# Kernel optimization log

Measured on AMD Instinct MI355X. Metric: run time of the kernel, lower is better.

The kernel has to match this reference:

```python
import jax, jax.numpy as jnp
import numpy as np


def setup_inputs() -> dict:
    key = jax.random.key(0)
    x = jax.random.normal(key, (32, 128, 112, 112), dtype=jnp.float32)
    return {"x": x}


def reference(x) -> jnp.ndarray:
    # Max-Feature-Map: pairwise max over adjacent channel pairs.
    # Equivalent to the original loop that takes max(x[:,k], x[:,k+1]) for k in 0,2,...
    B, C, H, W = x.shape
    return x.reshape(B, C // 2, 2, H, W).max(axis=2)  # [B, C/2, H, W]
```

## Files before the change

### kernel.cpp

```cpp
#include <hip/hip_runtime.h>


typedef float f32x4 __attribute__((ext_vector_type(4)));

static constexpr int P4 = (112 * 112) / 4;
static constexpr int N4_OUT = 32 * 64 * P4;

__global__ __launch_bounds__(256) void mfm_kernel(const f32x4* __restrict__ x,
                                                  f32x4* __restrict__ out) {
    int i = blockIdx.x * blockDim.x + threadIdx.x;
    int p = i / P4;
    int in0 = i + p * P4;
    f32x4 a = __builtin_nontemporal_load(&x[in0]);
    f32x4 b = __builtin_nontemporal_load(&x[in0 + P4]);
    f32x4 r;
    r.x = fmaxf(a.x, b.x);
    r.y = fmaxf(a.y, b.y);
    r.z = fmaxf(a.z, b.z);
    r.w = fmaxf(a.w, b.w);
    __builtin_nontemporal_store(r, &out[i]);
}

extern "C" void kernel_launch(void* const* d_in, const int* in_sizes, int n_in,
                              void* d_out, int out_size, void* d_ws, size_t ws_size,
                              hipStream_t stream) {
    const f32x4* x = (const f32x4*)d_in[0];
    f32x4* out = (f32x4*)d_out;
    constexpr int block = 256;
    constexpr int grid = N4_OUT / block;
    mfm_kernel<<<grid, block, 0, stream>>>(x, out);
}
```

Measured before the change: 287.2 us.

## Map one block per output plane with unrolled multi-load per thread

Each block now processes one whole output channel plane, 448 threads each doing seven float4 loads from both input channels before computing and storing. This removes the per-element integer division and gives each thread more loads in flight. The cost is fewer blocks (2048) with a larger register footprint, which may reduce occupancy and latency hiding.

After: 292.3 us. Within noise of the previous version (+1.8%).

```diff
diff --git a/kernel.cpp b/kernel.cpp
--- a/kernel.cpp
+++ b/kernel.cpp
@@ -4,21 +4,35 @@
 typedef float f32x4 __attribute__((ext_vector_type(4)));
 
 static constexpr int P4 = (112 * 112) / 4;
-static constexpr int N4_OUT = 32 * 64 * P4;
+static constexpr int NPLANES_OUT = 32 * 64;
+static constexpr int BLOCK = 448;
+static constexpr int ITERS = P4 / BLOCK;
 
-__global__ __launch_bounds__(256) void mfm_kernel(const f32x4* __restrict__ x,
-                                                  f32x4* __restrict__ out) {
-    int i = blockIdx.x * blockDim.x + threadIdx.x;
-    int p = i / P4;
-    int in0 = i + p * P4;
-    f32x4 a = __builtin_nontemporal_load(&x[in0]);
-    f32x4 b = __builtin_nontemporal_load(&x[in0 + P4]);
-    f32x4 r;
-    r.x = fmaxf(a.x, b.x);
-    r.y = fmaxf(a.y, b.y);
-    r.z = fmaxf(a.z, b.z);
-    r.w = fmaxf(a.w, b.w);
-    __builtin_nontemporal_store(r, &out[i]);
+__global__ __launch_bounds__(BLOCK) void mfm_kernel(const f32x4* __restrict__ x,
+                                                    f32x4* __restrict__ out) {
+    const int p = blockIdx.x;
+    const int t = threadIdx.x;
+
+    const f32x4* __restrict__ a = x + (size_t)(2 * p) * P4;
+    const f32x4* __restrict__ b = a + P4;
+    f32x4* __restrict__ o = out + (size_t)p * P4;
+
+    f32x4 va[ITERS], vb[ITERS];
+#pragma unroll
+    for (int k = 0; k < ITERS; ++k)
+        va[k] = __builtin_nontemporal_load(&a[t + BLOCK * k]);
+#pragma unroll
+    for (int k = 0; k < ITERS; ++k)
+        vb[k] = __builtin_nontemporal_load(&b[t + BLOCK * k]);
+#pragma unroll
+    for (int k = 0; k < ITERS; ++k) {
+        f32x4 r;
+        r.x = fmaxf(va[k].x, vb[k].x);
+        r.y = fmaxf(va[k].y, vb[k].y);
+        r.z = fmaxf(va[k].z, vb[k].z);
+        r.w = fmaxf(va[k].w, vb[k].w);
+        __builtin_nontemporal_store(r, &o[t + BLOCK * k]);
+    }
 }
 
 extern "C" void kernel_launch(void* const* d_in, const int* in_sizes, int n_in,
@@ -26,7 +40,5 @@
                               hipStream_t stream) {
     const f32x4* x = (const f32x4*)d_in[0];
     f32x4* out = (f32x4*)d_out;
-    constexpr int block = 256;
-    constexpr int grid = N4_OUT / block;
-    mfm_kernel<<<grid, block, 0, stream>>>(x, out);
+    mfm_kernel<<<NPLANES_OUT, BLOCK, 0, stream>>>(x, out);
 }
```
